# Performance work log

Hardware: AMD Instinct MI355X
Metric: run time of the kernel (lower is better)

The kernel has to match this reference:

```python
import math
import jax, jax.numpy as jnp
import numpy as np
from jax.scipy.special import xlogy, gammaln

WINDOW = 256  # window_size from init_kwargs


def get_positional_embed(seq_len, feature_size):
    # Enformer-style relative positional features; feature_size % 6 == 0.
    distances = jnp.arange(-seq_len + 1, seq_len, dtype=jnp.float32)  # (2W-1,)
    nb = feature_size // 6
    absd = jnp.abs(distances)[:, None]  # (2W-1, 1)
    # exponential basis
    max_range = math.log(seq_len) / math.log(2.0)
    half_life = 2.0 ** jnp.linspace(3.0, max_range, nb)
    feat_exp = jnp.exp(-math.log(2.0) / half_life[None, :] * absd)
    # central mask basis
    center_widths = 2.0 ** jnp.arange(1, nb + 1, dtype=jnp.float32) - 1.0
    feat_cm = (center_widths[None, :] > absd).astype(jnp.float32)
    # gamma pdf basis
    stddev = seq_len / (2.0 * nb)
    start_mean = seq_len / nb
    mean = jnp.linspace(start_mean, float(seq_len), nb)[None, :]
    concentration = (mean / stddev) ** 2
    rate = mean / stddev ** 2
    log_unnorm = xlogy(concentration - 1.0, absd) - rate * absd
    log_norm = gammaln(concentration) - concentration * jnp.log(rate)
    prob = jnp.exp(log_unnorm - log_norm) + 1e-8
    feat_gamma = prob / jnp.max(prob, axis=-1, keepdims=True)
    emb = jnp.concatenate([feat_exp, feat_cm, feat_gamma], axis=-1)
    return jnp.concatenate([emb, jnp.sign(distances)[:, None] * emb], axis=-1)  # (2W-1, F)


def relative_shift_swin(x):
    # x: (b, h, nw, t1, t2) with t2 = 2*t1 - 1  ->  (b, h, nw, t1, t1)
    b, h, w, t1, t2 = x.shape
    x = jnp.pad(x, ((0, 0), (0, 0), (0, 0), (0, 0), (1, 0)))  # pad zero at front of last dim
    x = x.reshape(b, h, w, t2 + 1, t1)
    x = x[:, :, :, 1:, :].reshape(b, h, w, t1, t2)
    return x[..., :(t2 + 1) // 2]


def setup_inputs() -> dict:
    key = jax.random.key(0)
    ks = jax.random.split(key, 7)
    B, N, C, H, D = 2, 8192, 768, 12, 64
    return {
        "x": jax.random.normal(ks[0], (B, N, C), jnp.float32),
        "w_qkv": jax.random.normal(ks[1], (C, 3 * H * D), jnp.float32) * 0.02,
        "w_out": jax.random.normal(ks[2], (H * D, C), jnp.float32) * 0.02,
        "b_out": jnp.zeros((C,), jnp.float32),
        "w_rel": jax.random.normal(ks[3], (C, H * D), jnp.float32) * 0.02,
        "rel_content_bias": jax.random.normal(ks[4], (1, H, 1, 1, D), jnp.float32),
        "rel_pos_bias": jax.random.normal(ks[5], (1, H, 1, 1, D), jnp.float32),
    }


def reference(x, w_qkv, w_out, b_out, w_rel, rel_content_bias, rel_pos_bias):
    b, n, c = x.shape
    H, D = rel_content_bias.shape[1], rel_content_bias.shape[-1]
    W = WINDOW
    nw = n // W  # n divisible by W (no padding branch)
    # qkv projection; output layout of to_qkv is (h, d, k) per 'b n (h d k) -> k b h n d'
    qkv = (x @ w_qkv).reshape(b, n, H, D, 3)
    q = jnp.transpose(qkv[..., 0], (0, 2, 1, 3)).reshape(b, H, nw, W, D)
    k = jnp.transpose(qkv[..., 1], (0, 2, 1, 3)).reshape(b, H, nw, W, D)
    v = jnp.transpose(qkv[..., 2], (0, 2, 1, 3)).reshape(b, H, nw, W, D)
    # relative position keys: 'n (h d) -> h n d'
    F = w_rel.shape[0]
    positions = get_positional_embed(W, F)  # (2W-1, F)
    rel_k = jnp.transpose((positions @ w_rel).reshape(2 * W - 1, H, D), (1, 0, 2))  # (H, 2W-1, D)
    # content attention (scaled); position attention (unscaled, as in source)
    content_attn = jnp.einsum('bhwid,bhwjd->bhwij', q + rel_content_bias, k) * (D ** -0.5)
    rel_logits = jnp.einsum('bhwid,hjd->bhwij', q + rel_pos_bias, rel_k)  # (b,H,nw,W,2W-1)
    position_attn = relative_shift_swin(rel_logits)  # (b,H,nw,W,W)
    attn = jax.nn.softmax(content_attn + position_attn, axis=-1)
    out = jnp.einsum('bhwij,bhwjd->bhwid', attn, v)  # (b,H,nw,W,D)
    out = jnp.transpose(out, (0, 2, 3, 1, 4)).reshape(b, nw, W, H * D)  # 'b h w n d -> b w n (h d)'
    out = out @ w_out + b_out
    return out.reshape(b, n, c)
```

## Files before the change

### kernel.cpp

```cpp
#include <hip/hip_runtime.h>
#include <math.h>

typedef __attribute__((ext_vector_type(8))) short bf8;
typedef __attribute__((ext_vector_type(4))) float f4;
typedef __attribute__((ext_vector_type(2))) unsigned u2;
typedef __attribute__((ext_vector_type(4))) unsigned u4;

__device__ __forceinline__ float bf2f(short s) {
    union { unsigned u; float f; } v; v.u = ((unsigned)(unsigned short)s) << 16; return v.f;
}
__device__ __forceinline__ short f2bf(float f) {
    return (short)((__float_as_uint(f) + 0x8000u) >> 16);
}
__device__ __forceinline__ unsigned pk2(float a, float b) {
    unsigned ua = __float_as_uint(a) + 0x8000u;
    unsigned ub = __float_as_uint(b) + 0x8000u;
    return __builtin_amdgcn_perm(ub, ua, 0x07060302u);
}
__device__ __forceinline__ void gload16(const short* g, short* l) {
    __builtin_amdgcn_global_load_lds(
        (const __attribute__((address_space(1))) void*)g,
        (__attribute__((address_space(3))) void*)l,
        16, 0, 0);
}

__global__ __launch_bounds__(256) void xb_k(const float* __restrict__ X, short* __restrict__ XB) {
    long idx = (long)blockIdx.x * 256 + threadIdx.x;
    const float* src = X + idx * 8;
    float4 v0 = *(const float4*)(src);
    float4 v1 = *(const float4*)(src + 4);
    u4 p; p.x = pk2(v0.x, v0.y); p.y = pk2(v0.z, v0.w);
    p.z = pk2(v1.x, v1.y); p.w = pk2(v1.z, v1.w);
    *(u4*)(XB + idx * 8) = p;
}

__global__ void pos_kernel(short* __restrict__ P) {
    const int row = blockIdx.x;
    const int j = threadIdx.x;
    if (row == 511) {
        for (int t = j; t < 768; t += 128) P[511 * 768 + t] = 0;
        return;
    }
    const double dist = (double)(row - 255);
    const double ad = fabs(dist);
    double hl = exp2(3.0 + 5.0 * (double)j / 127.0);
    double fe = exp(-M_LN2 / hl * ad);
    double cw = exp2((double)(j + 1)) - 1.0;
    double fc = (cw > ad) ? 1.0 : 0.0;
    double m = 2.0 + 2.0 * (double)j;
    double conc = m * m;
    double lun = (ad == 0.0) ? -INFINITY : (conc - 1.0) * log(ad);
    lun -= m * ad;
    double lnorm = lgamma(conc) - conc * log(m);
    double prob = exp(lun - lnorm) + 1e-8;
    __shared__ double red[128];
    red[j] = prob;
    __syncthreads();
    for (int s2 = 64; s2 > 0; s2 >>= 1) {
        if (j < s2) red[j] = fmax(red[j], red[j + s2]);
        __syncthreads();
    }
    double fg = prob / red[0];
    float sg = (dist > 0.0) ? 1.f : ((dist < 0.0) ? -1.f : 0.f);
    int base = row * 768;
    P[base + j]        = f2bf((float)fe);
    P[base + 128 + j]  = f2bf((float)fc);
    P[base + 256 + j]  = f2bf((float)fg);
    P[base + 384 + j]  = f2bf(sg * (float)fe);
    P[base + 512 + j]  = f2bf(sg * (float)fc);
    P[base + 640 + j]  = f2bf(sg * (float)fg);
}

__global__ void wT_k(const float* __restrict__ W, short* __restrict__ WT,
                     int K, int N) {
    int idx = blockIdx.x * 256 + threadIdx.x;
    int kq = K >> 2;
    if (idx >= N * kq) return;
    int n = idx / kq, k = (idx % kq) << 2;
    float a = W[(long)(k + 0) * N + n];
    float b = W[(long)(k + 1) * N + n];
    float c = W[(long)(k + 2) * N + n];
    float d = W[(long)(k + 3) * N + n];
    u2 r; r.x = pk2(a, b); r.y = pk2(c, d);
    *(u2*)(WT + (long)n * K + k) = r;
}

__global__ __launch_bounds__(256) void gemm_k(
    const short* __restrict__ A, const short* __restrict__ BT,
    int M, int N, int K, int mode,
    short* __restrict__ Cb, float* __restrict__ Cf, const float* __restrict__ bias,
    short* __restrict__ Qo, short* __restrict__ Ko, short* __restrict__ Vt)
{
    __shared__ __attribute__((aligned(16))) short As[128 * 64];
    __shared__ __attribute__((aligned(16))) short Bs[128 * 64];
    const int tid = threadIdx.x;
    const int lane = tid & 63;
    const int wave = tid >> 6;
    const int wm = wave >> 1, wn = wave & 1;
    const int c = lane & 15, quad = lane >> 4;
    const int m0 = blockIdx.x * 128, n0 = blockIdx.y * 128;
    const int lrow = lane >> 3;
    const int lslot = lane & 7;

    f4 acc[4][4];
#pragma unroll
    for (int i = 0; i < 4; ++i)
#pragma unroll
        for (int jx = 0; jx < 4; ++jx) acc[i][jx] = (f4){0.f, 0.f, 0.f, 0.f};

    for (int k0 = 0; k0 < K; k0 += 64) {
#pragma unroll
        for (int i = 0; i < 4; ++i) {
            int grp = wave * 4 + i;
            int row = grp * 8 + lrow;
            int slot = lslot ^ (row & 7);
            const short* src;
            if (mode == 2) {
                int m = m0 + row;
                src = A + (((long)((m >> 13) * 12 + (k0 >> 6)) * 8192 + (m & 8191)) * 64 + slot * 8);
            } else {
                src = A + (long)(m0 + row) * K + k0 + slot * 8;
            }
            gload16(src, &As[grp * 512]);
        }
#pragma unroll
        for (int i = 0; i < 4; ++i) {
            int grp = wave * 4 + i;
            int row = grp * 8 + lrow;
            int slot = lslot ^ (row & 7);
            const short* src = BT + (long)(n0 + row) * K + k0 + slot * 8;
            gload16(src, &Bs[grp * 512]);
        }
        __syncthreads();
#pragma unroll
        for (int ks = 0; ks < 2; ++ks) {
            bf8 a[4], b[4];
#pragma unroll
            for (int mt = 0; mt < 4; ++mt) {
                int row = wm * 64 + mt * 16 + c;
                int slot = (ks * 4 + quad) ^ (row & 7);
                a[mt] = *(const bf8*)(&As[row * 64 + slot * 8]);
            }
#pragma unroll
            for (int nt = 0; nt < 4; ++nt) {
                int row = wn * 64 + nt * 16 + c;
                int slot = (ks * 4 + quad) ^ (row & 7);
                b[nt] = *(const bf8*)(&Bs[row * 64 + slot * 8]);
            }
#pragma unroll
            for (int mt = 0; mt < 4; ++mt)
#pragma unroll
                for (int nt = 0; nt < 4; ++nt)
                    acc[mt][nt] = __builtin_amdgcn_mfma_f32_16x16x32_bf16(a[mt], b[nt], acc[mt][nt], 0, 0, 0);
        }
        __syncthreads();
    }
#pragma unroll
    for (int mt = 0; mt < 4; ++mt)
#pragma unroll
        for (int nt = 0; nt < 4; ++nt)
#pragma unroll
            for (int r = 0; r < 4; ++r) {
                int m = m0 + wm * 64 + mt * 16 + quad * 4 + r;
                int n = n0 + wn * 64 + nt * 16 + c;
                float val = acc[mt][nt][r];
                if (mode == 1) {
                    int sel = n % 3, hd = n / 3;
                    int h = hd >> 6, d = hd & 63;
                    int bb = m >> 13, nn = m & 8191;
                    if (sel == 2) {
                        long off = ((long)((bb * 12 + h) * 32 + (nn >> 8))) * 16384 + d * 256 + (nn & 255);
                        Vt[off] = f2bf(val);
                    } else {
                        long off = ((long)((bb * 12 + h) * 8192 + nn)) * 64 + d;
                        ((sel == 0) ? Qo : Ko)[off] = f2bf(val);
                    }
                } else if (mode == 2) {
                    Cf[(long)m * N + n] = val + bias[n];
                } else {
                    Cb[(long)m * N + n] = f2bf(val);
                }
            }
}

__global__ __launch_bounds__(256) void attn_k(
    short* __restrict__ Q, const short* __restrict__ Kk, const short* __restrict__ Vt,
    const short* __restrict__ RK,
    const float* __restrict__ rcb, const float* __restrict__ rpb)
{
    __shared__ __attribute__((aligned(16))) short Ks[256 * 64];
    __shared__ __attribute__((aligned(16))) short Ps[4][16 * 136];
    const int bid = blockIdx.x;
    const int low = bid & 7;
    const int strip = low >> 1;
    const int rest = bid >> 3;
    const int w = rest & 31;
    const int q_ = rest >> 5;
    const int h = ((q_ % 6) << 1) | (low & 1);
    const int b = q_ / 6;
    const int tid = threadIdx.x, lane = tid & 63, wave = tid >> 6;
    const int c = lane & 15, quad = lane >> 4;
    const int i0w = strip * 64 + wave * 16;

    const long base_bh = ((long)(b * 12 + h) * 8192 + (long)w * 256) * 64;
    short* Qh = Q + base_bh;
    const short* Kh = Kk + base_bh;
    const short* Vw = Vt + (((long)(b * 12 + h) * 32 + w) << 14);
    const short* RKh = RK + h * 64;

#pragma unroll
    for (int i = 0; i < 8; ++i) {
        int p = tid + i * 256;
        int row = p >> 3, ls = p & 7;
        gload16(Kh + row * 64 + (ls ^ (row & 7)) * 8, &Ks[(wave * 64 + i * 256) * 8]);
    }

    bf8 qc[2], qp[2];
#pragma unroll
    for (int ks = 0; ks < 2; ++ks) {
        bf8 qraw = *(const bf8*)(Qh + (i0w + c) * 64 + ks * 32 + quad * 8);
        float4 cb0 = *(const float4*)(rcb + h * 64 + ks * 32 + quad * 8);
        float4 cb1 = *(const float4*)(rcb + h * 64 + ks * 32 + quad * 8 + 4);
        float4 pb0 = *(const float4*)(rpb + h * 64 + ks * 32 + quad * 8);
        float4 pb1 = *(const float4*)(rpb + h * 64 + ks * 32 + quad * 8 + 4);
        float cbv[8] = {cb0.x, cb0.y, cb0.z, cb0.w, cb1.x, cb1.y, cb1.z, cb1.w};
        float pbv[8] = {pb0.x, pb0.y, pb0.z, pb0.w, pb1.x, pb1.y, pb1.z, pb1.w};
#pragma unroll
        for (int u = 0; u < 8; ++u) {
            float qv = bf2f(qraw[u]);
            qc[ks][u] = f2bf(qv + cbv[u]);
            qp[ks][u] = f2bf(qv + pbv[u]);
        }
    }

    const int r0 = 240 - i0w;
    bf8 rfb[2][2];
#pragma unroll
    for (int t = 0; t < 2; ++t)
#pragma unroll
        for (int ks = 0; ks < 2; ++ks)
            rfb[t][ks] = *(const bf8*)(RKh + (long)(r0 + t * 16 + c) * 768 + ks * 32 + quad * 8);

    __syncthreads();

    f4 S[16], R[17];
#pragma unroll
    for (int ct = 0; ct < 16; ++ct) S[ct] = (f4){0.f, 0.f, 0.f, 0.f};
#pragma unroll
    for (int rt = 0; rt < 17; ++rt) R[rt] = (f4){0.f, 0.f, 0.f, 0.f};
#pragma unroll
    for (int t = 0; t < 17; ++t) {
        bf8 cur0 = rfb[t & 1][0], cur1 = rfb[t & 1][1];
        if (t + 2 < 17) {
#pragma unroll
            for (int ks = 0; ks < 2; ++ks)
                rfb[t & 1][ks] = *(const bf8*)(RKh + (long)(r0 + (t + 2) * 16 + c) * 768 + ks * 32 + quad * 8);
        }
        if (t < 16) {
            int row = t * 16 + c;
#pragma unroll
            for (int ks = 0; ks < 2; ++ks) {
                bf8 kf = *(const bf8*)(&Ks[row * 64 + (((ks * 4 + quad) ^ (row & 7))) * 8]);
                S[t] = __builtin_amdgcn_mfma_f32_16x16x32_bf16(qc[ks], kf, S[t], 0, 0, 0);
            }
        }
        R[t] = __builtin_amdgcn_mfma_f32_16x16x32_bf16(qp[0], cur0, R[t], 0, 0, 0);
        R[t] = __builtin_amdgcn_mfma_f32_16x16x32_bf16(qp[1], cur1, R[t], 0, 0, 0);
    }
    __syncthreads();

    short* Vs = Ks;
#pragma unroll
    for (int i = 0; i < 8; ++i) {
        int p = tid + i * 256;
        int row = p >> 5, ls = p & 31;
        gload16(Vw + row * 256 + (ls ^ ((row & 7) << 2)) * 8, &Vs[(wave * 2 + i * 8) * 256]);
    }

#pragma unroll
    for (int ct = 0; ct < 16; ++ct)
#pragma unroll
        for (int r = 0; r < 4; ++r) {
            int ip = quad * 4 + r;
            int src = (lane & 48) | ((15 - ip + c) & 15);
            float vA = __shfl(R[ct][r], src);
            float vB = __shfl(R[ct + 1][r], src);
            float pos = (c <= ip) ? vA : vB;
            S[ct][r] = S[ct][r] * 0.125f + pos;
        }

    float mx[4] = {-3.4e38f, -3.4e38f, -3.4e38f, -3.4e38f};
#pragma unroll
    for (int ct = 0; ct < 16; ++ct)
#pragma unroll
        for (int r = 0; r < 4; ++r) mx[r] = fmaxf(mx[r], S[ct][r]);
#pragma unroll
    for (int r = 0; r < 4; ++r)
#pragma unroll
        for (int o = 1; o < 16; o <<= 1) mx[r] = fmaxf(mx[r], __shfl_xor(mx[r], o));
    float sm[4] = {0.f, 0.f, 0.f, 0.f};
#pragma unroll
    for (int ct = 0; ct < 16; ++ct)
#pragma unroll
        for (int r = 0; r < 4; ++r) {
            float p = __expf(S[ct][r] - mx[r]);
            S[ct][r] = p;
            sm[r] += p;
        }
#pragma unroll
    for (int r = 0; r < 4; ++r)
#pragma unroll
        for (int o = 1; o < 16; o <<= 1) sm[r] += __shfl_xor(sm[r], o);
    float inv[4];
#pragma unroll
    for (int r = 0; r < 4; ++r) inv[r] = 1.0f / sm[r];

    __syncthreads();

    f4 O[4];
#pragma unroll
    for (int vt = 0; vt < 4; ++vt) O[vt] = (f4){0.f, 0.f, 0.f, 0.f};
#pragma unroll
    for (int half = 0; half < 2; ++half) {
#pragma unroll
        for (int ct = 0; ct < 8; ++ct)
#pragma unroll
            for (int r = 0; r < 4; ++r)
                Ps[wave][(quad * 4 + r) * 136 + ct * 16 + c] = f2bf(S[half * 8 + ct][r] * inv[r]);
#pragma unroll
        for (int kt = 0; kt < 4; ++kt) {
            bf8 af = *(const bf8*)(&Ps[wave][c * 136 + kt * 32 + quad * 8]);
#pragma unroll
            for (int vt = 0; vt < 4; ++vt) {
                int row = vt * 16 + c;
                int slot = (((half * 4 + kt) * 4 + quad) ^ ((row & 7) << 2));
                bf8 bv = *(const bf8*)(&Vs[row * 256 + slot * 8]);
                O[vt] = __builtin_amdgcn_mfma_f32_16x16x32_bf16(af, bv, O[vt], 0, 0, 0);
            }
        }
    }
#pragma unroll
    for (int vt = 0; vt < 4; ++vt)
#pragma unroll
        for (int r = 0; r < 4; ++r)
            Qh[(i0w + quad * 4 + r) * 64 + vt * 16 + c] = f2bf(O[vt][r]);
}

extern "C" void kernel_launch(void* const* d_in, const int* in_sizes, int n_in,
                              void* d_out, int out_size, void* d_ws, size_t ws_size,
                              hipStream_t stream) {
    const float* x     = (const float*)d_in[0];
    const float* w_qkv = (const float*)d_in[1];
    const float* w_out = (const float*)d_in[2];
    const float* b_out = (const float*)d_in[3];
    const float* w_rel = (const float*)d_in[4];
    const float* rcb   = (const float*)d_in[5];
    const float* rpb   = (const float*)d_in[6];

    char* ws = (char*)d_ws;
    short* wqkvT = (short*)(ws);
    short* woutT = (short*)(ws + 3538944L);
    short* wrelT = (short*)(ws + 4718592L);
    short* pos   = (short*)(ws + 5898240L);
    short* relk  = (short*)(ws + 6684672L);
    short* q     = (short*)(ws + 7471104L);
    short* k     = (short*)(ws + 32636928L);
    short* vT    = (short*)(ws + 57802752L);
    short* xb    = (short*)d_out;

    wT_k<<<(2304 * 192 + 255) / 256, 256, 0, stream>>>(w_qkv, wqkvT, 768, 2304);
    wT_k<<<(768 * 192 + 255) / 256, 256, 0, stream>>>(w_out, woutT, 768, 768);
    wT_k<<<(768 * 192 + 255) / 256, 256, 0, stream>>>(w_rel, wrelT, 768, 768);
    pos_kernel<<<512, 128, 0, stream>>>(pos);
    xb_k<<<6144, 256, 0, stream>>>(x, xb);
    gemm_k<<<dim3(4, 6), 256, 0, stream>>>(pos, wrelT, 512, 768, 768, 0,
                                           relk, nullptr, nullptr, nullptr, nullptr, nullptr);
    gemm_k<<<dim3(128, 18), 256, 0, stream>>>(xb, wqkvT, 16384, 2304, 768, 1,
                                              nullptr, nullptr, nullptr, q, k, vT);
    attn_k<<<3072, 256, 0, stream>>>(q, k, vT, relk, rcb, rpb);
    gemm_k<<<dim3(128, 6), 256, 0, stream>>>(q, woutT, 16384, 768, 768, 2,
                                             nullptr, (float*)d_out, b_out, nullptr, nullptr, nullptr);
}
```

Baseline: 362.3 us.

## Enlarge GEMM tiles to 256x256 with double-buffered LDS K-pipeline

Rewrites the GEMM kernel to use 256x256 output tiles with 512 threads (8 waves), a K-step of 32, and a double-buffered LDS ping-pong so the next K slice loads while the current one is computed. The LDS swizzle changes to fit 32-wide rows, and the launch grids are adjusted to match. The goal is to raise arithmetic intensity and hide global-load latency. In exchange, the grids get much smaller (e.g. 64x9 blocks for QKV and 6 blocks for the rel-k GEMM), which can underfill the GPU's compute units, and each thread holds twice as many accumulator registers.

Measured after the change: 435.9 us. 1.2x slower.

```diff
diff --git a/kernel.cpp b/kernel.cpp
--- a/kernel.cpp
+++ b/kernel.cpp
@@ -85,83 +85,85 @@
     *(u2*)(WT + (long)n * K + k) = r;
 }
 
-__global__ __launch_bounds__(256) void gemm_k(
+__global__ __launch_bounds__(512, 2) void gemm_k(
     const short* __restrict__ A, const short* __restrict__ BT,
     int M, int N, int K, int mode,
     short* __restrict__ Cb, float* __restrict__ Cf, const float* __restrict__ bias,
     short* __restrict__ Qo, short* __restrict__ Ko, short* __restrict__ Vt)
 {
-    __shared__ __attribute__((aligned(16))) short As[128 * 64];
-    __shared__ __attribute__((aligned(16))) short Bs[128 * 64];
+    __shared__ __attribute__((aligned(16))) short lds[2][16384];
     const int tid = threadIdx.x;
     const int lane = tid & 63;
     const int wave = tid >> 6;
-    const int wm = wave >> 1, wn = wave & 1;
+    const int wm = wave >> 2, wn = wave & 3;
     const int c = lane & 15, quad = lane >> 4;
-    const int m0 = blockIdx.x * 128, n0 = blockIdx.y * 128;
-    const int lrow = lane >> 3;
-    const int lslot = lane & 7;
-
-    f4 acc[4][4];
-#pragma unroll
-    for (int i = 0; i < 4; ++i)
+    const int m0 = blockIdx.x * 256, n0 = blockIdx.y * 256;
+    const int lrow = lane >> 2;
+    const int lslot = lane & 3;
+
+    f4 acc[8][4];
+#pragma unroll
+    for (int i = 0; i < 8; ++i)
 #pragma unroll
         for (int jx = 0; jx < 4; ++jx) acc[i][jx] = (f4){0.f, 0.f, 0.f, 0.f};
 
-    for (int k0 = 0; k0 < K; k0 += 64) {
-#pragma unroll
-        for (int i = 0; i < 4; ++i) {
-            int grp = wave * 4 + i;
-            int row = grp * 8 + lrow;
-            int slot = lslot ^ (row & 7);
-            const short* src;
+    const int nT = K >> 5;
+
+    auto stage = [&](int buf, int k0) {
+        short* As = &lds[buf][0];
+        short* Bs = &lds[buf][8192];
+#pragma unroll
+        for (int i = 0; i < 2; ++i) {
+            int grp = wave * 2 + i;
+            int row = grp * 16 + lrow;
+            int ss = lslot ^ ((row >> 1) & 3);
+            const short* srcA;
             if (mode == 2) {
                 int m = m0 + row;
-                src = A + (((long)((m >> 13) * 12 + (k0 >> 6)) * 8192 + (m & 8191)) * 64 + slot * 8);
+                srcA = A + (((long)((m >> 13) * 12 + (k0 >> 6)) * 8192 + (m & 8191)) * 64
+                            + (k0 & 63) + ss * 8);
             } else {
-                src = A + (long)(m0 + row) * K + k0 + slot * 8;
+                srcA = A + (long)(m0 + row) * K + k0 + ss * 8;
             }
-            gload16(src, &As[grp * 512]);
-        }
-#pragma unroll
-        for (int i = 0; i < 4; ++i) {
-            int grp = wave * 4 + i;
-            int row = grp * 8 + lrow;
-            int slot = lslot ^ (row & 7);
-            const short* src = BT + (long)(n0 + row) * K + k0 + slot * 8;
-            gload16(src, &Bs[grp * 512]);
+            gload16(srcA, &As[grp * 512]);
+            const short* srcB = BT + (long)(n0 + row) * K + k0 + ss * 8;
+            gload16(srcB, &Bs[grp * 512]);
+        }
+    };
+
+    stage(0, 0);
+    __syncthreads();
+
+    for (int t = 0, cur = 0; t < nT; ++t, cur ^= 1) {
+        if (t + 1 < nT) stage(cur ^ 1, (t + 1) << 5);
+        const short* As = &lds[cur][0];
+        const short* Bs = &lds[cur][8192];
+        bf8 b[4];
+#pragma unroll
+        for (int nt = 0; nt < 4; ++nt) {
+            int row = wn * 64 + nt * 16 + c;
+            int slot = quad ^ ((row >> 1) & 3);
+            b[nt] = *(const bf8*)(&Bs[row * 32 + slot * 8]);
+        }
+#pragma unroll
+        for (int mt = 0; mt < 8; ++mt) {
+            int row = wm * 128 + mt * 16 + c;
+            int slot = quad ^ ((row >> 1) & 3);
+            bf8 a = *(const bf8*)(&As[row * 32 + slot * 8]);
+#pragma unroll
+            for (int nt = 0; nt < 4; ++nt)
+                acc[mt][nt] = __builtin_amdgcn_mfma_f32_16x16x32_bf16(a, b[nt], acc[mt][nt], 0, 0, 0);
         }
         __syncthreads();
-#pragma unroll
-        for (int ks = 0; ks < 2; ++ks) {
-            bf8 a[4], b[4];
-#pragma unroll
-            for (int mt = 0; mt < 4; ++mt) {
-                int row = wm * 64 + mt * 16 + c;
-                int slot = (ks * 4 + quad) ^ (row & 7);
-                a[mt] = *(const bf8*)(&As[row * 64 + slot * 8]);
-            }
-#pragma unroll
-            for (int nt = 0; nt < 4; ++nt) {
-                int row = wn * 64 + nt * 16 + c;
-                int slot = (ks * 4 + quad) ^ (row & 7);
-                b[nt] = *(const bf8*)(&Bs[row * 64 + slot * 8]);
-            }
-#pragma unroll
-            for (int mt = 0; mt < 4; ++mt)
-#pragma unroll
-                for (int nt = 0; nt < 4; ++nt)
-                    acc[mt][nt] = __builtin_amdgcn_mfma_f32_16x16x32_bf16(a[mt], b[nt], acc[mt][nt], 0, 0, 0);
-        }
-        __syncthreads();
-    }
-#pragma unroll
-    for (int mt = 0; mt < 4; ++mt)
+    }
+
+#pragma unroll
+    for (int mt = 0; mt < 8; ++mt)
 #pragma unroll
         for (int nt = 0; nt < 4; ++nt)
 #pragma unroll
             for (int r = 0; r < 4; ++r) {
-                int m = m0 + wm * 64 + mt * 16 + quad * 4 + r;
+                int m = m0 + wm * 128 + mt * 16 + quad * 4 + r;
                 int n = n0 + wn * 64 + nt * 16 + c;
                 float val = acc[mt][nt][r];
                 if (mode == 1) {
@@ -373,11 +375,11 @@
     wT_k<<<(768 * 192 + 255) / 256, 256, 0, stream>>>(w_rel, wrelT, 768, 768);
     pos_kernel<<<512, 128, 0, stream>>>(pos);
     xb_k<<<6144, 256, 0, stream>>>(x, xb);
-    gemm_k<<<dim3(4, 6), 256, 0, stream>>>(pos, wrelT, 512, 768, 768, 0,
+    gemm_k<<<dim3(2, 3), 512, 0, stream>>>(pos, wrelT, 512, 768, 768, 0,
                                            relk, nullptr, nullptr, nullptr, nullptr, nullptr);
-    gemm_k<<<dim3(128, 18), 256, 0, stream>>>(xb, wqkvT, 16384, 2304, 768, 1,
-                                              nullptr, nullptr, nullptr, q, k, vT);
+    gemm_k<<<dim3(64, 9), 512, 0, stream>>>(xb, wqkvT, 16384, 2304, 768, 1,
+                                            nullptr, nullptr, nullptr, q, k, vT);
     attn_k<<<3072, 256, 0, stream>>>(q, k, vT, relk, rcb, rpb);
-    gemm_k<<<dim3(128, 6), 256, 0, stream>>>(q, woutT, 16384, 768, 768, 2,
-                                             nullptr, (float*)d_out, b_out, nullptr, nullptr, nullptr);
-}
+    gemm_k<<<dim3(64, 3), 512, 0, stream>>>(q, woutT, 16384, 768, 768, 2,
+                                            nullptr, (float*)d_out, b_out, nullptr, nullptr, nullptr);
+}
```
